# Kernel optimization log

Hardware: AMD Instinct MI355X
Metric: run time of the kernel (lower is better)

The kernel has to match this reference:

```python
import jax, jax.numpy as jnp
import numpy as np

F_IN = 22 * 1000   # flattened EEG trial
D_DENSE = 100      # Dense(100) -> becomes T=100 timesteps of dim 1
H = 128            # LSTM units
N_CLASS = 4


def setup_inputs() -> dict:
    key = jax.random.key(0)
    ks = jax.random.split(key, 8)
    B = 4096
    s1 = 1.0 / np.sqrt(F_IN)
    sr = 1.0 / np.sqrt(H)
    x = jax.random.normal(ks[0], (B, 22, 1000), dtype=jnp.float32)
    W1 = jax.random.uniform(ks[1], (F_IN, D_DENSE), jnp.float32, -s1, s1)
    b1 = jnp.zeros((D_DENSE,), jnp.float32)
    # Keras LSTM kernels: input kernel [1, 4H], recurrent kernel [H, 4H], bias [4H]
    Wk = jax.random.uniform(ks[2], (1, 4 * H), jnp.float32, -1.0, 1.0)
    Wr = jax.random.normal(ks[3], (H, 4 * H), dtype=jnp.float32) * sr
    # Keras unit_forget_bias: f-gate bias initialized to 1
    bl = jnp.concatenate([jnp.zeros(H), jnp.ones(H), jnp.zeros(2 * H)]).astype(jnp.float32)
    W2 = jax.random.uniform(ks[4], (H, N_CLASS), jnp.float32, -sr, sr)
    b2 = jnp.zeros((N_CLASS,), jnp.float32)
    return {"x": x, "W1": W1, "b1": b1, "Wk": Wk, "Wr": Wr, "bl": bl, "W2": W2, "b2": b2}


def _lstm_last(seq, Wk, Wr, bl):
    # seq: [B, T, 1]; returns final hidden state [B, H]
    B = seq.shape[0]
    # precompute input contribution for all steps: [T, B, 4H]
    zx = jnp.einsum('btf,fg->tbg', seq, Wk) + bl

    def step(carry, zxt):
        h, c = carry
        z = zxt + h @ Wr                      # [B, 4H]
        i, f, g, o = jnp.split(z, 4, axis=-1)  # keras gate order: i, f, c, o
        i = jax.nn.sigmoid(i)
        f = jax.nn.sigmoid(f)
        g = jnp.tanh(g)
        o = jax.nn.sigmoid(o)
        c = f * c + i * g
        h = o * jnp.tanh(c)
        return (h, c), None

    init = (jnp.zeros((B, H), seq.dtype), jnp.zeros((B, H), seq.dtype))
    (h, _), _ = jax.lax.scan(step, init, zx)
    return h


def reference(x, W1, b1, Wk, Wr, bl, W2, b2):
    B = x.shape[0]
    flat = x.reshape(B, -1)                 # Flatten
    d = flat @ W1 + b1                      # Dense(100), linear activation
    seq = d.reshape(B, D_DENSE, 1)          # Reshape((100, 1))
    h = _lstm_last(seq, Wk, Wr, bl)         # LSTM(128) -> last hidden state
    logits = h @ W2 + b2                    # Dense(4)
    return jax.nn.softmax(logits, axis=-1)
```

## Files before the change

### kernel.cpp

```cpp
#include <hip/hip_runtime.h>
#include <stdint.h>

#define F_IN   22000
#define B_SZ   4096
#define T_STEPS 100
#define NSPLIT 16
#define NCHUNK 22
#define KSPAN  (NCHUNK * 64)
#define ACC_STRIDE 104
#define ACCB_BYTES ((size_t)B_SZ * ACC_STRIDE * 4)
#define BIMG_BYTES 28672
#define BIMG_HALF  14336
#define W1IMG_BYTES ((size_t)NSPLIT * NCHUNK * BIMG_BYTES)
#define WRIMG_BYTES (128 * 1024)

typedef float f32x4 __attribute__((ext_vector_type(4)));
typedef short s16x8 __attribute__((ext_vector_type(8)));

__device__ inline unsigned short f2bf(float f){
  unsigned u = __builtin_bit_cast(unsigned, f);
  u += 0x7FFFu + ((u >> 16) & 1u);
  return (unsigned short)(u >> 16);
}
__device__ inline float bf2f(unsigned short h){
  return __builtin_bit_cast(float, ((unsigned)h) << 16);
}
__device__ inline float sigf(float x){
  return __builtin_amdgcn_rcpf(1.f + __expf(-x));
}
__device__ inline float tanhf_(float x){
  return 1.f - 2.f * __builtin_amdgcn_rcpf(__expf(2.f * x) + 1.f);
}

__global__ __launch_bounds__(256) void k_zero(float4* __restrict__ p, int n4){
  int i = blockIdx.x * 256 + threadIdx.x;
  if (i < n4) p[i] = make_float4(0.f, 0.f, 0.f, 0.f);
}

__global__ __launch_bounds__(256) void k_w1img(const float* __restrict__ W1,
                                               char* __restrict__ img){
  __shared__ float tile[64][129];
  int ch = blockIdx.x, s = blockIdx.y;
  int k0 = s * KSPAN + ch * 64;
  char* base = img + ((size_t)(s * NCHUNK + ch)) * BIMG_BYTES;
  int tid = threadIdx.x;
  for (int idx = tid; idx < 64 * 128; idx += 256){
    int k = idx >> 7, c = idx & 127;
    float v = 0.f;
    if (c < 100 && (k0 + k) < F_IN) v = W1[(size_t)(k0 + k) * 100 + c];
    tile[k][c] = v;
  }
  __syncthreads();
  #pragma unroll
  for (int q = 0; q < 4; ++q){
    int task = q * 256 + tid;
    if (task < 896){
      int p  = task * 16;
      int c  = p >> 7;
      int k8 = ((p >> 4) & 7) ^ (c & 7);
      unsigned hw[4], lw[4];
      #pragma unroll
      for (int jj = 0; jj < 4; ++jj){
        float v0 = tile[k8 * 8 + jj * 2][c];
        float v1 = tile[k8 * 8 + jj * 2 + 1][c];
        unsigned short h0 = f2bf(v0), l0 = f2bf(v0 - bf2f(h0));
        unsigned short h1 = f2bf(v1), l1 = f2bf(v1 - bf2f(h1));
        hw[jj] = (unsigned)h0 | ((unsigned)h1 << 16);
        lw[jj] = (unsigned)l0 | ((unsigned)l1 << 16);
      }
      *(uint4*)(base + p)             = make_uint4(hw[0], hw[1], hw[2], hw[3]);
      *(uint4*)(base + BIMG_HALF + p) = make_uint4(lw[0], lw[1], lw[2], lw[3]);
    }
  }
}

__global__ __launch_bounds__(256) void k_wrimg(const float* __restrict__ Wr,
                                               char* __restrict__ wrimg){
  int gid = blockIdx.x * 256 + threadIdx.x;
  int lane = gid & 63, slot = gid >> 6;
  int kk = slot & 3, G = (slot >> 2) & 3, w = slot >> 4;
  int oct = lane >> 4, lr = lane & 15;
  int col = G * 128 + w * 16 + lr;
  unsigned pk[4];
  #pragma unroll
  for (int jj = 0; jj < 4; ++jj){
    float v0 = Wr[(size_t)(kk * 32 + oct * 8 + jj * 2)     * 512 + col];
    float v1 = Wr[(size_t)(kk * 32 + oct * 8 + jj * 2 + 1) * 512 + col];
    pk[jj] = (unsigned)f2bf(v0) | ((unsigned)f2bf(v1) << 16);
  }
  *(uint4*)(wrimg + (size_t)gid * 16) = make_uint4(pk[0], pk[1], pk[2], pk[3]);
}

__global__ __launch_bounds__(256, 2) void k_dense(const float* __restrict__ x,
                                                  const char* __restrict__ img,
                                                  float* __restrict__ accb){
  __shared__ char Bb0[BIMG_BYTES], Bb1[BIMG_BYTES];
  int tid = threadIdx.x;
  int lane = tid & 63, w = tid >> 6;
  int r = lane & 15, oct = lane >> 4;
  int brow = blockIdx.x * 128;
  int s = blockIdx.y;
  int arow0 = brow + w * 32 + r;
  const float* xrow0 = x + (size_t)arow0 * F_IN;
  const float* xrow1 = xrow0 + (size_t)16 * F_IN;
  const char* isrc = img + (size_t)s * NCHUNK * BIMG_BYTES;
  int kbase = s * KSPAN;

  f32x4 acc0[7], acc1[7];
  #pragma unroll
  for (int i = 0; i < 7; ++i){ acc0[i] = (f32x4)0.f; acc1[i] = (f32x4)0.f; }

  float4 xa0, xa1, xa2, xa3, xb0, xb1, xb2, xb3;
  float4 ya0, ya1, ya2, ya3, yb0, yb1, yb2, yb3;

#define ALOAD(CH, A0, A1, A2, A3, B0, B1, B2, B3) do{                        \
    int k0_ = kbase + (CH) * 64;                                             \
    int ka0_ = k0_ + oct * 8;                                                \
    int ka1_ = k0_ + 32 + oct * 8;                                           \
    A0 = make_float4(0.f,0.f,0.f,0.f); A1 = A0; A2 = A0; A3 = A0;            \
    B0 = A0; B1 = A0; B2 = A0; B3 = A0;                                      \
    if (ka0_ < F_IN){ A0 = *(const float4*)(xrow0 + ka0_);                   \
                      A1 = *(const float4*)(xrow0 + ka0_ + 4);               \
                      B0 = *(const float4*)(xrow1 + ka0_);                   \
                      B1 = *(const float4*)(xrow1 + ka0_ + 4); }             \
    if (ka1_ < F_IN){ A2 = *(const float4*)(xrow0 + ka1_);                   \
                      A3 = *(const float4*)(xrow0 + ka1_ + 4);               \
                      B2 = *(const float4*)(xrow1 + ka1_);                   \
                      B3 = *(const float4*)(xrow1 + ka1_ + 4); }             \
  }while(0)

#define STAGE(CH, BUF) do{                                                   \
    const char* src_ = isrc + (size_t)(CH) * BIMG_BYTES;                     \
    _Pragma("unroll")                                                        \
    for (int i_ = 0; i_ < 7; ++i_){                                          \
      int seg_ = i_ * 4 + w;                                                 \
      __builtin_amdgcn_global_load_lds(                                      \
        (const __attribute__((address_space(1))) void*)(src_ + seg_ * 1024 + lane * 16), \
        (__attribute__((address_space(3))) void*)((BUF) + seg_ * 1024), 16, 0, 0); \
    }                                                                        \
  }while(0)

#define CONV16(VA, H0, L0, H1, L1) do{                                       \
    _Pragma("unroll")                                                        \
    for (int j_ = 0; j_ < 8; ++j_){                                          \
      unsigned short h_ = f2bf(VA[j_]);                                      \
      H0[j_] = (short)h_; L0[j_] = (short)f2bf(VA[j_] - bf2f(h_));           \
    }                                                                        \
    _Pragma("unroll")                                                        \
    for (int j_ = 0; j_ < 8; ++j_){                                          \
      unsigned short h_ = f2bf(VA[8 + j_]);                                  \
      H1[j_] = (short)h_; L1[j_] = (short)f2bf(VA[8 + j_] - bf2f(h_));       \
    }                                                                        \
  }while(0)

#define CONVMFMA(BUF, A0, A1, A2, A3, B0, B1, B2, B3) do{                    \
    float va_[16] = {A0.x,A0.y,A0.z,A0.w, A1.x,A1.y,A1.z,A1.w,               \
                     A2.x,A2.y,A2.z,A2.w, A3.x,A3.y,A3.z,A3.w};              \
    float vb_[16] = {B0.x,B0.y,B0.z,B0.w, B1.x,B1.y,B1.z,B1.w,               \
                     B2.x,B2.y,B2.z,B2.w, B3.x,B3.y,B3.z,B3.w};              \
    s16x8 pah0_, pal0_, pah1_, pal1_, qah0_, qal0_, qah1_, qal1_;            \
    CONV16(va_, pah0_, pal0_, pah1_, pal1_);                                 \
    CONV16(vb_, qah0_, qal0_, qah1_, qal1_);                                 \
    _Pragma("unroll")                                                        \
    for (int ct_ = 0; ct_ < 7; ++ct_){                                       \
      int c_ = ct_ * 16 + r;                                                 \
      int byte0_ = ((c_ * 128 + oct * 16) ^ ((c_ & 7) << 4));                \
      int byte1_ = ((c_ * 128 + 64 + oct * 16) ^ ((c_ & 7) << 4));           \
      s16x8 bh0_ = *(s16x8*)((BUF) + byte0_);                                \
      s16x8 bl0_ = *(s16x8*)((BUF) + BIMG_HALF + byte0_);                    \
      s16x8 bh1_ = *(s16x8*)((BUF) + byte1_);                                \
      s16x8 bl1_ = *(s16x8*)((BUF) + BIMG_HALF + byte1_);                    \
      acc0[ct_] = __builtin_amdgcn_mfma_f32_16x16x32_bf16(pah0_, bh0_, acc0[ct_], 0, 0, 0); \
      acc0[ct_] = __builtin_amdgcn_mfma_f32_16x16x32_bf16(pah0_, bl0_, acc0[ct_], 0, 0, 0); \
      acc0[ct_] = __builtin_amdgcn_mfma_f32_16x16x32_bf16(pal0_, bh0_, acc0[ct_], 0, 0, 0); \
      acc0[ct_] = __builtin_amdgcn_mfma_f32_16x16x32_bf16(pah1_, bh1_, acc0[ct_], 0, 0, 0); \
      acc0[ct_] = __builtin_amdgcn_mfma_f32_16x16x32_bf16(pah1_, bl1_, acc0[ct_], 0, 0, 0); \
      acc0[ct_] = __builtin_amdgcn_mfma_f32_16x16x32_bf16(pal1_, bh1_, acc0[ct_], 0, 0, 0); \
      acc1[ct_] = __builtin_amdgcn_mfma_f32_16x16x32_bf16(qah0_, bh0_, acc1[ct_], 0, 0, 0); \
      acc1[ct_] = __builtin_amdgcn_mfma_f32_16x16x32_bf16(qah0_, bl0_, acc1[ct_], 0, 0, 0); \
      acc1[ct_] = __builtin_amdgcn_mfma_f32_16x16x32_bf16(qal0_, bh0_, acc1[ct_], 0, 0, 0); \
      acc1[ct_] = __builtin_amdgcn_mfma_f32_16x16x32_bf16(qah1_, bh1_, acc1[ct_], 0, 0, 0); \
      acc1[ct_] = __builtin_amdgcn_mfma_f32_16x16x32_bf16(qah1_, bl1_, acc1[ct_], 0, 0, 0); \
      acc1[ct_] = __builtin_amdgcn_mfma_f32_16x16x32_bf16(qal1_, bh1_, acc1[ct_], 0, 0, 0); \
    }                                                                        \
  }while(0)

  ALOAD(0, xa0, xa1, xa2, xa3, xb0, xb1, xb2, xb3);
  STAGE(0, Bb0);
  __syncthreads();

  for (int ch = 0; ch < NCHUNK; ch += 2){
    if (ch + 1 < NCHUNK){
      ALOAD(ch + 1, ya0, ya1, ya2, ya3, yb0, yb1, yb2, yb3);
      STAGE(ch + 1, Bb1);
    }
    CONVMFMA(Bb0, xa0, xa1, xa2, xa3, xb0, xb1, xb2, xb3);
    __syncthreads();
    if (ch + 1 < NCHUNK){
      if (ch + 2 < NCHUNK){
        ALOAD(ch + 2, xa0, xa1, xa2, xa3, xb0, xb1, xb2, xb3);
        STAGE(ch + 2, Bb0);
      }
      CONVMFMA(Bb1, ya0, ya1, ya2, ya3, yb0, yb1, yb2, yb3);
      __syncthreads();
    }
  }

#undef ALOAD
#undef STAGE
#undef CONV16
#undef CONVMFMA

  #pragma unroll
  for (int ct = 0; ct < 7; ++ct){
    int col = ct * 16 + r;
    if (col < 100){
      #pragma unroll
      for (int reg = 0; reg < 4; ++reg){
        int orow0 = brow + w * 32 + oct * 4 + reg;
        atomicAdd(&accb[(size_t)orow0 * ACC_STRIDE + col], acc0[ct][reg]);
        atomicAdd(&accb[(size_t)(orow0 + 16) * ACC_STRIDE + col], acc1[ct][reg]);
      }
    }
  }
}

__global__ __launch_bounds__(512, 2) void k_lstm(const float* __restrict__ accb,
                                                 const float* __restrict__ b1,
                                                 const float* __restrict__ Wk,
                                                 const char* __restrict__ wrimg,
                                                 const float* __restrict__ bl,
                                                 const float* __restrict__ W2,
                                                 const float* __restrict__ b2,
                                                 float* __restrict__ out){
  __shared__ unsigned short hbuf[2][16 * 128];
  __shared__ float dld[16][ACC_STRIDE];
  __shared__ float hf[16][132];
  int tid = threadIdx.x;
  int lane = tid & 63, w = tid >> 6;
  int oct = lane >> 4, lr = lane & 15;
  int brow = blockIdx.x * 16;

  for (int i = tid; i < 2048; i += 512) hbuf[0][i] = 0;
  for (int i = tid; i < 16 * T_STEPS; i += 512){
    int r = i / T_STEPS, t = i % T_STEPS;
    dld[r][t] = accb[(size_t)(brow + r) * ACC_STRIDE + t] + b1[t];
  }

  float wkv[4], blv[4];
  s16x8 bfrag[4][4];
  #pragma unroll
  for (int G = 0; G < 4; ++G){
    int col = G * 128 + w * 16 + lr;
    wkv[G] = Wk[col];
    blv[G] = bl[col];
    #pragma unroll
    for (int kk = 0; kk < 4; ++kk){
      bfrag[G][kk] = *(const s16x8*)(wrimg +
          ((size_t)(((w * 4 + G) * 4 + kk) * 64 + lane)) * 16);
    }
  }
  float cst[4];
  #pragma unroll
  for (int reg = 0; reg < 4; ++reg) cst[reg] = 0.f;
  __syncthreads();

  for (int t = 0; t < T_STEPS; ++t){
    int cur = t & 1;
    f32x4 acc[4];
    float dv[4];
    #pragma unroll
    for (int reg = 0; reg < 4; ++reg) dv[reg] = dld[oct * 4 + reg][t];
    #pragma unroll
    for (int G = 0; G < 4; ++G)
      #pragma unroll
      for (int reg = 0; reg < 4; ++reg)
        acc[G][reg] = dv[reg] * wkv[G] + blv[G];
    #pragma unroll
    for (int kk = 0; kk < 4; ++kk){
      int abyte = (lr * 256 + kk * 64 + oct * 16) ^ ((lr & 7) << 4);
      s16x8 a = *(s16x8*)((char*)hbuf[cur] + abyte);
      #pragma unroll
      for (int G = 0; G < 4; ++G)
        acc[G] = __builtin_amdgcn_mfma_f32_16x16x32_bf16(a, bfrag[G][kk], acc[G], 0, 0, 0);
    }
    #pragma unroll
    for (int reg = 0; reg < 4; ++reg){
      float iv = sigf(acc[0][reg]);
      float fv = sigf(acc[1][reg]);
      float gv = tanhf_(acc[2][reg]);
      float ov = sigf(acc[3][reg]);
      float cv = fv * cst[reg] + iv * gv;
      cst[reg] = cv;
      float hv = ov * tanhf_(cv);
      int row = oct * 4 + reg;
      int col = w * 16 + lr;
      int byte = (row * 256 + col * 2) ^ ((row & 7) << 4);
      *(unsigned short*)((char*)hbuf[cur ^ 1] + byte) = f2bf(hv);
      if (t == T_STEPS - 1) hf[row][col] = hv;
    }
    __syncthreads();
  }

  if (tid < 64){
    int row = tid >> 2, cl = tid & 3;
    float a = b2[cl];
    #pragma unroll 8
    for (int j = 0; j < 128; ++j) a += hf[row][j] * W2[j * 4 + cl];
    float m = fmaxf(a, __shfl_xor(a, 1));
    m = fmaxf(m, __shfl_xor(m, 2));
    float e = __expf(a - m);
    float se = e + __shfl_xor(e, 1);
    se += __shfl_xor(se, 2);
    out[(size_t)(brow + row) * 4 + cl] = e * __builtin_amdgcn_rcpf(se);
  }
}

extern "C" void kernel_launch(void* const* d_in, const int* in_sizes, int n_in,
                              void* d_out, int out_size, void* d_ws, size_t ws_size,
                              hipStream_t stream){
  const float* x  = (const float*)d_in[0];
  const float* W1 = (const float*)d_in[1];
  const float* b1 = (const float*)d_in[2];
  const float* Wk = (const float*)d_in[3];
  const float* Wr = (const float*)d_in[4];
  const float* bl = (const float*)d_in[5];
  const float* W2 = (const float*)d_in[6];
  const float* b2 = (const float*)d_in[7];
  float* out = (float*)d_out;

  float* accb  = (float*)d_ws;
  char*  img   = (char*)d_ws + ACCB_BYTES;
  char*  wrimg = (char*)d_ws + ACCB_BYTES + W1IMG_BYTES;
  const int n4 = B_SZ * ACC_STRIDE / 4;

  k_zero<<<(n4 + 255) / 256, 256, 0, stream>>>((float4*)accb, n4);
  k_w1img<<<dim3(NCHUNK, NSPLIT), 256, 0, stream>>>(W1, img);
  k_wrimg<<<32, 256, 0, stream>>>(Wr, wrimg);
  k_dense<<<dim3(B_SZ / 128, NSPLIT), 256, 0, stream>>>(x, img, accb);
  k_lstm<<<B_SZ / 16, 512, 0, stream>>>(accb, b1, Wk, wrimg, bl, W2, b2, out);
}
```

Measured before the change: 238.4 us.

## Pre-swizzle W1 image into MFMA fragment order and load B directly from global

The W1 bf16 hi/lo image is rewritten so that each 16-byte lane slot matches the MFMA B-fragment layout. The dense kernel then reads B fragments straight from global/L2 into registers instead of staging them through LDS with global_load_lds. This removes the LDS buffers and all block barriers from the main loop and software-pipelines the per-column-tile loads against the MFMAs. The cost is that every wave re-reads the weight image from cache instead of sharing one LDS copy, which adds global memory traffic and latency exposure.

```diff
diff --git a/kernel.cpp b/kernel.cpp
--- a/kernel.cpp
+++ b/kernel.cpp
@@ -10,7 +10,6 @@
 #define ACC_STRIDE 104
 #define ACCB_BYTES ((size_t)B_SZ * ACC_STRIDE * 4)
 #define BIMG_BYTES 28672
-#define BIMG_HALF  14336
 #define W1IMG_BYTES ((size_t)NSPLIT * NCHUNK * BIMG_BYTES)
 #define WRIMG_BYTES (128 * 1024)
 
@@ -52,25 +51,25 @@
   }
   __syncthreads();
   #pragma unroll
-  for (int q = 0; q < 4; ++q){
-    int task = q * 256 + tid;
-    if (task < 896){
-      int p  = task * 16;
-      int c  = p >> 7;
-      int k8 = ((p >> 4) & 7) ^ (c & 7);
-      unsigned hw[4], lw[4];
-      #pragma unroll
-      for (int jj = 0; jj < 4; ++jj){
-        float v0 = tile[k8 * 8 + jj * 2][c];
-        float v1 = tile[k8 * 8 + jj * 2 + 1][c];
-        unsigned short h0 = f2bf(v0), l0 = f2bf(v0 - bf2f(h0));
-        unsigned short h1 = f2bf(v1), l1 = f2bf(v1 - bf2f(h1));
-        hw[jj] = (unsigned)h0 | ((unsigned)h1 << 16);
-        lw[jj] = (unsigned)l0 | ((unsigned)l1 << 16);
-      }
-      *(uint4*)(base + p)             = make_uint4(hw[0], hw[1], hw[2], hw[3]);
-      *(uint4*)(base + BIMG_HALF + p) = make_uint4(lw[0], lw[1], lw[2], lw[3]);
-    }
+  for (int q = 0; q < 7; ++q){
+    int t = q * 256 + tid;
+    int lane = t & 63, frag = t >> 6;
+    int ct = frag >> 2, sub = frag & 3;
+    int half = sub >> 1, hilo = sub & 1;
+    int c  = ct * 16 + (lane & 15);
+    int kb = half * 32 + (lane >> 4) * 8;
+    unsigned pk[4];
+    #pragma unroll
+    for (int jj = 0; jj < 4; ++jj){
+      float v0 = tile[kb + jj * 2][c];
+      float v1 = tile[kb + jj * 2 + 1][c];
+      unsigned short h0 = f2bf(v0), l0 = f2bf(v0 - bf2f(h0));
+      unsigned short h1 = f2bf(v1), l1 = f2bf(v1 - bf2f(h1));
+      unsigned short e0 = hilo ? l0 : h0;
+      unsigned short e1 = hilo ? l1 : h1;
+      pk[jj] = (unsigned)e0 | ((unsigned)e1 << 16);
+    }
+    *(uint4*)(base + (size_t)t * 16) = make_uint4(pk[0], pk[1], pk[2], pk[3]);
   }
 }
 
@@ -94,7 +93,6 @@
 __global__ __launch_bounds__(256, 2) void k_dense(const float* __restrict__ x,
                                                   const char* __restrict__ img,
                                                   float* __restrict__ accb){
-  __shared__ char Bb0[BIMG_BYTES], Bb1[BIMG_BYTES];
   int tid = threadIdx.x;
   int lane = tid & 63, w = tid >> 6;
   int r = lane & 15, oct = lane >> 4;
@@ -103,7 +101,7 @@
   int arow0 = brow + w * 32 + r;
   const float* xrow0 = x + (size_t)arow0 * F_IN;
   const float* xrow1 = xrow0 + (size_t)16 * F_IN;
-  const char* isrc = img + (size_t)s * NCHUNK * BIMG_BYTES;
+  const char* isrc = img + (size_t)s * NCHUNK * BIMG_BYTES + (size_t)lane * 16;
   int kbase = s * KSPAN;
 
   f32x4 acc0[7], acc1[7];
@@ -129,15 +127,12 @@
                       B3 = *(const float4*)(xrow1 + ka1_ + 4); }             \
   }while(0)
 
-#define STAGE(CH, BUF) do{                                                   \
-    const char* src_ = isrc + (size_t)(CH) * BIMG_BYTES;                     \
-    _Pragma("unroll")                                                        \
-    for (int i_ = 0; i_ < 7; ++i_){                                          \
-      int seg_ = i_ * 4 + w;                                                 \
-      __builtin_amdgcn_global_load_lds(                                      \
-        (const __attribute__((address_space(1))) void*)(src_ + seg_ * 1024 + lane * 16), \
-        (__attribute__((address_space(3))) void*)((BUF) + seg_ * 1024), 16, 0, 0); \
-    }                                                                        \
+#define LDB(CH, CT, F0, F1, F2, F3) do{                                      \
+    const char* b_ = isrc + (size_t)(CH) * BIMG_BYTES + (CT) * 4096;         \
+    F0 = *(const s16x8*)(b_);                                                \
+    F1 = *(const s16x8*)(b_ + 1024);                                         \
+    F2 = *(const s16x8*)(b_ + 2048);                                         \
+    F3 = *(const s16x8*)(b_ + 3072);                                         \
   }while(0)
 
 #define CONV16(VA, H0, L0, H1, L1) do{                                       \
@@ -153,7 +148,21 @@
     }                                                                        \
   }while(0)
 
-#define CONVMFMA(BUF, A0, A1, A2, A3, B0, B1, B2, B3) do{                    \
+#define MFMA_CT(CT, BH0, BL0, BH1, BL1)                                      \
+    acc0[CT] = __builtin_amdgcn_mfma_f32_16x16x32_bf16(pah0_, BH0, acc0[CT], 0, 0, 0); \
+    acc0[CT] = __builtin_amdgcn_mfma_f32_16x16x32_bf16(pah0_, BL0, acc0[CT], 0, 0, 0); \
+    acc0[CT] = __builtin_amdgcn_mfma_f32_16x16x32_bf16(pal0_, BH0, acc0[CT], 0, 0, 0); \
+    acc0[CT] = __builtin_amdgcn_mfma_f32_16x16x32_bf16(pah1_, BH1, acc0[CT], 0, 0, 0); \
+    acc0[CT] = __builtin_amdgcn_mfma_f32_16x16x32_bf16(pah1_, BL1, acc0[CT], 0, 0, 0); \
+    acc0[CT] = __builtin_amdgcn_mfma_f32_16x16x32_bf16(pal1_, BH1, acc0[CT], 0, 0, 0); \
+    acc1[CT] = __builtin_amdgcn_mfma_f32_16x16x32_bf16(qah0_, BH0, acc1[CT], 0, 0, 0); \
+    acc1[CT] = __builtin_amdgcn_mfma_f32_16x16x32_bf16(qah0_, BL0, acc1[CT], 0, 0, 0); \
+    acc1[CT] = __builtin_amdgcn_mfma_f32_16x16x32_bf16(qal0_, BH0, acc1[CT], 0, 0, 0); \
+    acc1[CT] = __builtin_amdgcn_mfma_f32_16x16x32_bf16(qah1_, BH1, acc1[CT], 0, 0, 0); \
+    acc1[CT] = __builtin_amdgcn_mfma_f32_16x16x32_bf16(qah1_, BL1, acc1[CT], 0, 0, 0); \
+    acc1[CT] = __builtin_amdgcn_mfma_f32_16x16x32_bf16(qal1_, BH1, acc1[CT], 0, 0, 0);
+
+#define COMPUTE(CH, A0, A1, A2, A3, B0, B1, B2, B3) do{                      \
     float va_[16] = {A0.x,A0.y,A0.z,A0.w, A1.x,A1.y,A1.z,A1.w,               \
                      A2.x,A2.y,A2.z,A2.w, A3.x,A3.y,A3.z,A3.w};              \
     float vb_[16] = {B0.x,B0.y,B0.z,B0.w, B1.x,B1.y,B1.z,B1.w,               \
@@ -161,55 +170,33 @@
     s16x8 pah0_, pal0_, pah1_, pal1_, qah0_, qal0_, qah1_, qal1_;            \
     CONV16(va_, pah0_, pal0_, pah1_, pal1_);                                 \
     CONV16(vb_, qah0_, qal0_, qah1_, qal1_);                                 \
-    _Pragma("unroll")                                                        \
-    for (int ct_ = 0; ct_ < 7; ++ct_){                                       \
-      int c_ = ct_ * 16 + r;                                                 \
-      int byte0_ = ((c_ * 128 + oct * 16) ^ ((c_ & 7) << 4));                \
-      int byte1_ = ((c_ * 128 + 64 + oct * 16) ^ ((c_ & 7) << 4));           \
-      s16x8 bh0_ = *(s16x8*)((BUF) + byte0_);                                \
-      s16x8 bl0_ = *(s16x8*)((BUF) + BIMG_HALF + byte0_);                    \
-      s16x8 bh1_ = *(s16x8*)((BUF) + byte1_);                                \
-      s16x8 bl1_ = *(s16x8*)((BUF) + BIMG_HALF + byte1_);                    \
-      acc0[ct_] = __builtin_amdgcn_mfma_f32_16x16x32_bf16(pah0_, bh0_, acc0[ct_], 0, 0, 0); \
-      acc0[ct_] = __builtin_amdgcn_mfma_f32_16x16x32_bf16(pah0_, bl0_, acc0[ct_], 0, 0, 0); \
-      acc0[ct_] = __builtin_amdgcn_mfma_f32_16x16x32_bf16(pal0_, bh0_, acc0[ct_], 0, 0, 0); \
-      acc0[ct_] = __builtin_amdgcn_mfma_f32_16x16x32_bf16(pah1_, bh1_, acc0[ct_], 0, 0, 0); \
-      acc0[ct_] = __builtin_amdgcn_mfma_f32_16x16x32_bf16(pah1_, bl1_, acc0[ct_], 0, 0, 0); \
-      acc0[ct_] = __builtin_amdgcn_mfma_f32_16x16x32_bf16(pal1_, bh1_, acc0[ct_], 0, 0, 0); \
-      acc1[ct_] = __builtin_amdgcn_mfma_f32_16x16x32_bf16(qah0_, bh0_, acc1[ct_], 0, 0, 0); \
-      acc1[ct_] = __builtin_amdgcn_mfma_f32_16x16x32_bf16(qah0_, bl0_, acc1[ct_], 0, 0, 0); \
-      acc1[ct_] = __builtin_amdgcn_mfma_f32_16x16x32_bf16(qal0_, bh0_, acc1[ct_], 0, 0, 0); \
-      acc1[ct_] = __builtin_amdgcn_mfma_f32_16x16x32_bf16(qah1_, bh1_, acc1[ct_], 0, 0, 0); \
-      acc1[ct_] = __builtin_amdgcn_mfma_f32_16x16x32_bf16(qah1_, bl1_, acc1[ct_], 0, 0, 0); \
-      acc1[ct_] = __builtin_amdgcn_mfma_f32_16x16x32_bf16(qal1_, bh1_, acc1[ct_], 0, 0, 0); \
-    }                                                                        \
+    s16x8 u0_, u1_, u2_, u3_, v0_, v1_, v2_, v3_;                            \
+    LDB(CH, 0, u0_, u1_, u2_, u3_);                                          \
+    LDB(CH, 1, v0_, v1_, v2_, v3_);  MFMA_CT(0, u0_, u1_, u2_, u3_);         \
+    LDB(CH, 2, u0_, u1_, u2_, u3_);  MFMA_CT(1, v0_, v1_, v2_, v3_);         \
+    LDB(CH, 3, v0_, v1_, v2_, v3_);  MFMA_CT(2, u0_, u1_, u2_, u3_);         \
+    LDB(CH, 4, u0_, u1_, u2_, u3_);  MFMA_CT(3, v0_, v1_, v2_, v3_);         \
+    LDB(CH, 5, v0_, v1_, v2_, v3_);  MFMA_CT(4, u0_, u1_, u2_, u3_);         \
+    LDB(CH, 6, u0_, u1_, u2_, u3_);  MFMA_CT(5, v0_, v1_, v2_, v3_);         \
+    MFMA_CT(6, u0_, u1_, u2_, u3_);                                          \
   }while(0)
 
   ALOAD(0, xa0, xa1, xa2, xa3, xb0, xb1, xb2, xb3);
-  STAGE(0, Bb0);
-  __syncthreads();
-
   for (int ch = 0; ch < NCHUNK; ch += 2){
-    if (ch + 1 < NCHUNK){
+    if (ch + 1 < NCHUNK)
       ALOAD(ch + 1, ya0, ya1, ya2, ya3, yb0, yb1, yb2, yb3);
-      STAGE(ch + 1, Bb1);
-    }
-    CONVMFMA(Bb0, xa0, xa1, xa2, xa3, xb0, xb1, xb2, xb3);
-    __syncthreads();
-    if (ch + 1 < NCHUNK){
-      if (ch + 2 < NCHUNK){
-        ALOAD(ch + 2, xa0, xa1, xa2, xa3, xb0, xb1, xb2, xb3);
-        STAGE(ch + 2, Bb0);
-      }
-      CONVMFMA(Bb1, ya0, ya1, ya2, ya3, yb0, yb1, yb2, yb3);
-      __syncthreads();
-    }
+    COMPUTE(ch, xa0, xa1, xa2, xa3, xb0, xb1, xb2, xb3);
+    if (ch + 2 < NCHUNK)
+      ALOAD(ch + 2, xa0, xa1, xa2, xa3, xb0, xb1, xb2, xb3);
+    if (ch + 1 < NCHUNK)
+      COMPUTE(ch + 1, ya0, ya1, ya2, ya3, yb0, yb1, yb2, yb3);
   }
 
 #undef ALOAD
-#undef STAGE
+#undef LDB
 #undef CONV16
-#undef CONVMFMA
+#undef MFMA_CT
+#undef COMPUTE
 
   #pragma unroll
   for (int ct = 0; ct < 7; ++ct){
```

New measurement: 267.6 us. 1.12x slower.
